# Kernel optimization log

Measured on AMD Instinct MI355X. Metric: run time of the kernel, lower is better.

Reference implementation:

```python
import jax, jax.numpy as jnp
import numpy as np

N = 262144      # active coordinates
M = 131072      # rulebook entries per kernel offset
C_IN = 64
C_OUT = 64


def setup_inputs() -> dict:
    key = jax.random.key(0)
    k1, k2, k3, k4 = jax.random.split(key, 4)
    coords = jax.random.randint(k1, (N, 3), 0, 512, dtype=jnp.int64) if jax.config.jax_enable_x64 else jax.random.randint(k1, (N, 3), 0, 512, dtype=jnp.int32)
    feats = jax.random.normal(k2, (N, C_IN), dtype=jnp.float32)
    in_rows = jax.random.randint(k3, (9, M), 0, N, dtype=jnp.int32)
    out_rows = jax.random.randint(k4, (9, M), 0, N, dtype=jnp.int32)
    # weight init matches torch: randn * (1/sqrt(in_ch))
    weight = jax.random.normal(jax.random.fold_in(key, 5), (9, C_IN, C_OUT), dtype=jnp.float32) * (1.0 / C_IN ** 0.5)
    bias = jnp.zeros((C_OUT,), dtype=jnp.float32)
    return {"coords": coords, "feats": feats, "in_rows": in_rows,
            "out_rows": out_rows, "weight": weight, "bias": bias}


def reference(coords, feats, in_rows, out_rows, weight, bias):
    # Gather input features for all 9 kernel offsets: [9, M, C_in]
    gathered = feats[in_rows]
    # Per-offset GEMM: [9, M, C_out]
    prod = jnp.einsum('kmi,kio->kmo', gathered, weight)
    # Scatter-add into output rows
    out = jnp.zeros((feats.shape[0], weight.shape[2]), dtype=feats.dtype)
    out = out.at[out_rows.reshape(-1)].add(prod.reshape(-1, weight.shape[2]))
    out = out + bias
    return (coords, out)
```

## Files before the change

kernel.cpp:

```cpp
#include <hip/hip_runtime.h>
#include <hip/hip_bf16.h>

#define NPTS 262144
#define MRB  131072
#define KOFF 9

typedef __attribute__((ext_vector_type(8))) short short8;
typedef __attribute__((ext_vector_type(4))) float f32x4;

__device__ __forceinline__ short f2bf(float f) {
    __hip_bfloat16 h = __float2bfloat16(f);
    return __builtin_bit_cast(short, h);
}

__device__ __forceinline__ void atomic_add_f32(float* p, float v) {
    __hip_atomic_fetch_add(p, v, __ATOMIC_RELAXED, __HIP_MEMORY_SCOPE_AGENT);
}

__global__ __launch_bounds__(256) void init_kernel(const int* __restrict__ coords,
                                                   const float* __restrict__ bias,
                                                   float* __restrict__ out) {
    const int tid = blockIdx.x * blockDim.x + threadIdx.x;
    const int nc4 = (NPTS * 3) / 4;
    const int nf4 = (NPTS * 64) / 4;
    for (int i = tid; i < nc4 + nf4; i += gridDim.x * blockDim.x) {
        if (i < nc4) {
            int4 c = ((const int4*)coords)[i];
            float4 f;
            f.x = (float)c.x; f.y = (float)c.y; f.z = (float)c.z; f.w = (float)c.w;
            ((float4*)out)[i] = f;
        } else {
            int j = i - nc4;
            float4 b = ((const float4*)bias)[j & 15];
            ((float4*)(out + (size_t)NPTS * 3))[j] = b;
        }
    }
}

__global__ __launch_bounds__(256) void conv_main(const float* __restrict__ feats,
                                                 const int*   __restrict__ in_rows,
                                                 const int*   __restrict__ out_rows,
                                                 const float* __restrict__ weight,
                                                 float*       __restrict__ out) {
    const int lane = threadIdx.x & 63;
    const int wv   = threadIdx.x >> 6;
    const int lrow = lane & 15;
    const int lhi  = lane >> 4;
    const int BPK  = MRB / 64;
    const int k    = blockIdx.x / BPK;
    const int mb   = (blockIdx.x % BPK) * 64 + wv * 16;

    const float* Wk = weight + k * 64 * 64;
    short8 bfrag[2][4];
#pragma unroll
    for (int kk = 0; kk < 2; ++kk)
#pragma unroll
        for (int nt = 0; nt < 4; ++nt)
#pragma unroll
            for (int j = 0; j < 8; ++j)
                bfrag[kk][nt][j] = f2bf(Wk[(kk * 32 + lhi * 8 + j) * 64 + nt * 16 + lrow]);

    const int arow = in_rows[k * MRB + mb + lrow];
    const float* ap = feats + (long)arow * 64 + lhi * 8;

    f32x4 acc[4] = {};
#pragma unroll
    for (int kk = 0; kk < 2; ++kk) {
        float4 f0 = *(const float4*)(ap + kk * 32);
        float4 f1 = *(const float4*)(ap + kk * 32 + 4);
        short8 afrag;
        afrag[0] = f2bf(f0.x); afrag[1] = f2bf(f0.y);
        afrag[2] = f2bf(f0.z); afrag[3] = f2bf(f0.w);
        afrag[4] = f2bf(f1.x); afrag[5] = f2bf(f1.y);
        afrag[6] = f2bf(f1.z); afrag[7] = f2bf(f1.w);
#pragma unroll
        for (int nt = 0; nt < 4; ++nt)
            acc[nt] = __builtin_amdgcn_mfma_f32_16x16x32_bf16(afrag, bfrag[kk][nt], acc[nt], 0, 0, 0);
    }

    const int ob = k * MRB + mb + lhi * 4;
#pragma unroll
    for (int r = 0; r < 4; ++r) {
        const int orow = out_rows[ob + r];
        float* op = out + (long)orow * 64 + lrow;
#pragma unroll
        for (int nt = 0; nt < 4; ++nt)
            atomic_add_f32(op + nt * 16, acc[nt][r]);
    }
}

extern "C" void kernel_launch(void* const* d_in, const int* in_sizes, int n_in,
                              void* d_out, int out_size, void* d_ws, size_t ws_size,
                              hipStream_t stream) {
    const int*   coords   = (const int*)  d_in[0];
    const float* feats    = (const float*)d_in[1];
    const int*   in_rows  = (const int*)  d_in[2];
    const int*   out_rows = (const int*)  d_in[3];
    const float* weight   = (const float*)d_in[4];
    const float* bias     = (const float*)d_in[5];
    float* out = (float*)d_out;

    hipLaunchKernelGGL(init_kernel, dim3(2048), dim3(256), 0, stream, coords, bias, out);
    hipLaunchKernelGGL(conv_main, dim3(KOFF * (MRB / 64)), dim3(256), 0, stream,
                       feats, in_rows, out_rows, weight, out + (size_t)NPTS * 3);
}
```

Measured before the change: 364.2 us.

## Replace float atomic scatter with counting-sort bucketing and segmented reduction

```diff
diff --git a/kernel.cpp b/kernel.cpp
--- a/kernel.cpp
+++ b/kernel.cpp
@@ -4,22 +4,182 @@
 #define NPTS 262144
 #define MRB  131072
 #define KOFF 9
+#define NENT (KOFF * MRB)
 
 typedef __attribute__((ext_vector_type(8))) short short8;
+typedef __attribute__((ext_vector_type(4))) short short4v;
 typedef __attribute__((ext_vector_type(4))) float f32x4;
 
 __device__ __forceinline__ short f2bf(float f) {
     __hip_bfloat16 h = __float2bfloat16(f);
     return __builtin_bit_cast(short, h);
 }
-
+__device__ __forceinline__ float bf2f(unsigned short u) {
+    unsigned int x = ((unsigned int)u) << 16;
+    return __builtin_bit_cast(float, x);
+}
 __device__ __forceinline__ void atomic_add_f32(float* p, float v) {
     __hip_atomic_fetch_add(p, v, __ATOMIC_RELAXED, __HIP_MEMORY_SCOPE_AGENT);
 }
 
-__global__ __launch_bounds__(256) void init_kernel(const int* __restrict__ coords,
-                                                   const float* __restrict__ bias,
-                                                   float* __restrict__ out) {
+#define PROD_OFF   0ull
+#define POS_OFF    150994944ull
+#define START_OFF  155713536ull
+#define CURSOR_OFF 156762368ull
+#define COUNTS_OFF 157810944ull
+#define BSUM_OFF   158859520ull
+#define WS_NEED    158860544ull
+
+
+__global__ __launch_bounds__(256) void init_fast(const int* __restrict__ coords,
+                                                 float* __restrict__ out,
+                                                 int* __restrict__ counts) {
+    const int i = blockIdx.x * 256 + threadIdx.x;
+    const int nc4 = (NPTS * 3) / 4;
+    if (i < nc4) {
+        int4 c = ((const int4*)coords)[i];
+        float4 f;
+        f.x = (float)c.x; f.y = (float)c.y; f.z = (float)c.z; f.w = (float)c.w;
+        ((float4*)out)[i] = f;
+    } else {
+        int j = i - nc4;
+        ((int4*)counts)[j] = make_int4(0, 0, 0, 0);
+    }
+}
+
+__global__ __launch_bounds__(256) void hist_kernel(const int* __restrict__ out_rows,
+                                                   int* __restrict__ counts) {
+    const int e = blockIdx.x * 256 + threadIdx.x;
+    atomicAdd(&counts[out_rows[e]], 1);
+}
+
+__global__ __launch_bounds__(1024) void scan_blocks(const int* __restrict__ counts,
+                                                    int* __restrict__ start,
+                                                    int* __restrict__ bsum) {
+    __shared__ int lds[1024];
+    const int tid = threadIdx.x;
+    const int gid = blockIdx.x * 1024 + tid;
+    int v = counts[gid];
+    lds[tid] = v;
+    __syncthreads();
+#pragma unroll
+    for (int off = 1; off < 1024; off <<= 1) {
+        int t = (tid >= off) ? lds[tid - off] : 0;
+        __syncthreads();
+        lds[tid] += t;
+        __syncthreads();
+    }
+    start[gid] = lds[tid] - v;
+    if (tid == 1023) bsum[blockIdx.x] = lds[tid];
+}
+
+__global__ __launch_bounds__(256) void scan_bsum(int* __restrict__ bsum) {
+    __shared__ int lds[256];
+    const int tid = threadIdx.x;
+    int v = bsum[tid];
+    lds[tid] = v;
+    __syncthreads();
+#pragma unroll
+    for (int off = 1; off < 256; off <<= 1) {
+        int t = (tid >= off) ? lds[tid - off] : 0;
+        __syncthreads();
+        lds[tid] += t;
+        __syncthreads();
+    }
+    bsum[tid] = lds[tid] - v;
+}
+
+__global__ __launch_bounds__(1024) void add_offsets(int* __restrict__ start,
+                                                    const int* __restrict__ bsum,
+                                                    int* __restrict__ cursor) {
+    const int gid = blockIdx.x * 1024 + threadIdx.x;
+    int s = start[gid] + bsum[blockIdx.x];
+    start[gid] = s;
+    cursor[gid] = s;
+    if (gid == 0) start[NPTS] = NENT;
+}
+
+__global__ __launch_bounds__(256) void fill_pos(const int* __restrict__ out_rows,
+                                                int* __restrict__ cursor,
+                                                int* __restrict__ pos) {
+    const int e = blockIdx.x * 256 + threadIdx.x;
+    pos[e] = atomicAdd(&cursor[out_rows[e]], 1);
+}
+
+__global__ __launch_bounds__(256) void conv_prod(const float* __restrict__ feats,
+                                                 const int*   __restrict__ in_rows,
+                                                 const float* __restrict__ weight,
+                                                 const int*   __restrict__ pos,
+                                                 short*       __restrict__ prod) {
+    const int lane = threadIdx.x & 63;
+    const int wv   = threadIdx.x >> 6;
+    const int lrow = lane & 15;
+    const int lhi  = lane >> 4;
+    const int BPK  = MRB / 64;
+    const int k    = blockIdx.x / BPK;
+    const int mb   = (blockIdx.x % BPK) * 64 + wv * 16;
+
+    const float* Wk = weight + k * 64 * 64;
+    short8 wfrag[2][4];
+#pragma unroll
+    for (int kk = 0; kk < 2; ++kk)
+#pragma unroll
+        for (int mt = 0; mt < 4; ++mt)
+#pragma unroll
+            for (int j = 0; j < 8; ++j)
+                wfrag[kk][mt][j] = f2bf(Wk[(kk * 32 + lhi * 8 + j) * 64 + mt * 16 + lrow]);
+
+    const int e    = k * MRB + mb + lrow;
+    const int arow = in_rows[e];
+    const float* ap = feats + (long)arow * 64 + lhi * 8;
+
+    f32x4 acc[4] = {};
+#pragma unroll
+    for (int kk = 0; kk < 2; ++kk) {
+        float4 f0 = *(const float4*)(ap + kk * 32);
+        float4 f1 = *(const float4*)(ap + kk * 32 + 4);
+        short8 ffrag;
+        ffrag[0] = f2bf(f0.x); ffrag[1] = f2bf(f0.y);
+        ffrag[2] = f2bf(f0.z); ffrag[3] = f2bf(f0.w);
+        ffrag[4] = f2bf(f1.x); ffrag[5] = f2bf(f1.y);
+        ffrag[6] = f2bf(f1.z); ffrag[7] = f2bf(f1.w);
+#pragma unroll
+        for (int mt = 0; mt < 4; ++mt)
+            acc[mt] = __builtin_amdgcn_mfma_f32_16x16x32_bf16(wfrag[kk][mt], ffrag, acc[mt], 0, 0, 0);
+    }
+
+    const int p = pos[e];
+    short* pp = prod + (size_t)p * 64 + lhi * 4;
+#pragma unroll
+    for (int mt = 0; mt < 4; ++mt) {
+        short4v s;
+        s[0] = f2bf(acc[mt][0]); s[1] = f2bf(acc[mt][1]);
+        s[2] = f2bf(acc[mt][2]); s[3] = f2bf(acc[mt][3]);
+        *(short4v*)(pp + mt * 16) = s;
+    }
+}
+
+__global__ __launch_bounds__(256) void reduce_out(const short* __restrict__ prod,
+                                                  const int*   __restrict__ start,
+                                                  const float* __restrict__ bias,
+                                                  float*       __restrict__ out) {
+    const int lane = threadIdx.x & 63;
+    const int wid  = (blockIdx.x * 256 + threadIdx.x) >> 6;
+    const int nw   = (gridDim.x * 256) >> 6;
+    const float b  = bias[lane];
+    for (int r = wid; r < NPTS; r += nw) {
+        const int s0 = start[r], s1 = start[r + 1];
+        float acc = 0.f;
+        const unsigned short* p = (const unsigned short*)prod + (size_t)s0 * 64 + lane;
+        for (int s = s0; s < s1; ++s, p += 64)
+            acc += bf2f(*p);
+        out[(size_t)r * 64 + lane] = acc + b;
+    }
+}
+
+__global__ __launch_bounds__(256) void init_full(const int* __restrict__ coords,
+                                                 const float* __restrict__ bias,
+                                                 float* __restrict__ out) {
     const int tid = blockIdx.x * blockDim.x + threadIdx.x;
     const int nc4 = (NPTS * 3) / 4;
     const int nf4 = (NPTS * 64) / 4;
@@ -37,11 +197,11 @@
     }
 }
 
-__global__ __launch_bounds__(256) void conv_main(const float* __restrict__ feats,
-                                                 const int*   __restrict__ in_rows,
-                                                 const int*   __restrict__ out_rows,
-                                                 const float* __restrict__ weight,
-                                                 float*       __restrict__ out) {
+__global__ __launch_bounds__(256) void conv_atomic(const float* __restrict__ feats,
+                                                   const int*   __restrict__ in_rows,
+                                                   const int*   __restrict__ out_rows,
+                                                   const float* __restrict__ weight,
+                                                   float*       __restrict__ out) {
     const int lane = threadIdx.x & 63;
     const int wv   = threadIdx.x >> 6;
     const int lrow = lane & 15;
@@ -98,9 +258,30 @@
     const int*   out_rows = (const int*)  d_in[3];
     const float* weight   = (const float*)d_in[4];
     const float* bias     = (const float*)d_in[5];
-    float* out = (float*)d_out;
-
-    hipLaunchKernelGGL(init_kernel, dim3(2048), dim3(256), 0, stream, coords, bias, out);
-    hipLaunchKernelGGL(conv_main, dim3(KOFF * (MRB / 64)), dim3(256), 0, stream,
-                       feats, in_rows, out_rows, weight, out + (size_t)NPTS * 3);
-}
+    float* out      = (float*)d_out;
+    float* out_feat = out + (size_t)NPTS * 3;
+
+    if (ws_size >= WS_NEED) {
+        char* ws = (char*)d_ws;
+        short* prod  = (short*)(ws + PROD_OFF);
+        int* pos     = (int*)(ws + POS_OFF);
+        int* start   = (int*)(ws + START_OFF);
+        int* cursor  = (int*)(ws + CURSOR_OFF);
+        int* counts  = (int*)(ws + COUNTS_OFF);
+        int* bsum    = (int*)(ws + BSUM_OFF);
+
+        hipLaunchKernelGGL(init_fast,   dim3(1024), dim3(256),  0, stream, coords, out, counts);
+        hipLaunchKernelGGL(hist_kernel, dim3(NENT / 256), dim3(256), 0, stream, out_rows, counts);
+        hipLaunchKernelGGL(scan_blocks, dim3(NPTS / 1024), dim3(1024), 0, stream, counts, start, bsum);
+        hipLaunchKernelGGL(scan_bsum,   dim3(1),    dim3(256),  0, stream, bsum);
+        hipLaunchKernelGGL(add_offsets, dim3(NPTS / 1024), dim3(1024), 0, stream, start, bsum, cursor);
+        hipLaunchKernelGGL(fill_pos,    dim3(NENT / 256), dim3(256), 0, stream, out_rows, cursor, pos);
+        hipLaunchKernelGGL(conv_prod,   dim3(KOFF * (MRB / 64)), dim3(256), 0, stream,
+                           feats, in_rows, weight, pos, prod);
+        hipLaunchKernelGGL(reduce_out,  dim3(2048), dim3(256),  0, stream, prod, start, bias, out_feat);
+    } else {
+        hipLaunchKernelGGL(init_full,  dim3(2048), dim3(256), 0, stream, coords, bias, out);
+        hipLaunchKernelGGL(conv_atomic, dim3(KOFF * (MRB / 64)), dim3(256), 0, stream,
+                           feats, in_rows, out_rows, weight, out_feat);
+    }
+}
```

After: 439.8 us. 20.8% more time.

## Accumulate scatter in fp16 workspace with packed atomics and pre-converted bf16 inputs

Applied to the files above, without the earlier changes.

```diff
diff --git a/kernel.cpp b/kernel.cpp
--- a/kernel.cpp
+++ b/kernel.cpp
@@ -4,22 +4,140 @@
 #define NPTS 262144
 #define MRB  131072
 #define KOFF 9
+#define NENT (KOFF * MRB)
 
 typedef __attribute__((ext_vector_type(8))) short short8;
+typedef __attribute__((ext_vector_type(4))) short short4v;
 typedef __attribute__((ext_vector_type(4))) float f32x4;
+typedef _Float16 f16;
+typedef __attribute__((ext_vector_type(2))) _Float16 half2v;
+typedef __attribute__((ext_vector_type(4))) _Float16 f16x4;
 
 __device__ __forceinline__ short f2bf(float f) {
     __hip_bfloat16 h = __float2bfloat16(f);
     return __builtin_bit_cast(short, h);
 }
-
 __device__ __forceinline__ void atomic_add_f32(float* p, float v) {
     __hip_atomic_fetch_add(p, v, __ATOMIC_RELAXED, __HIP_MEMORY_SCOPE_AGENT);
 }
 
-__global__ __launch_bounds__(256) void init_kernel(const int* __restrict__ coords,
-                                                   const float* __restrict__ bias,
-                                                   float* __restrict__ out) {
+#if __has_builtin(__builtin_amdgcn_global_atomic_fadd_v2f16)
+typedef __attribute__((address_space(1))) half2v ghalf2;
+__device__ __forceinline__ void atomic_pk_add(f16* p, float x, float y) {
+    half2v v = {(f16)x, (f16)y};
+    __builtin_amdgcn_global_atomic_fadd_v2f16((ghalf2*)p, v);
+}
+#else
+__device__ __forceinline__ void atomic_pk_add(f16* p, float x, float y) {
+    half2v v = {(f16)x, (f16)y};
+    asm volatile("global_atomic_pk_add_f16 %0, %1, off" :: "v"(p), "v"(v) : "memory");
+}
+#endif
+
+#define FB_OFF   0ull
+#define WBF_OFF  33554432ull
+#define ACC_OFF  33628160ull
+#define ACC_BYTES 33554432ull
+#define WS_NEED  67182592ull
+
+
+__global__ __launch_bounds__(256) void prep(const int*   __restrict__ coords,
+                                            const float* __restrict__ feats,
+                                            const float* __restrict__ weight,
+                                            float* __restrict__ out,
+                                            short* __restrict__ fb,
+                                            short* __restrict__ wbf) {
+    const int T0 = (NPTS * 3) / 4;
+    const int T1 = T0 + NPTS * 16;
+    const int T2 = T1 + (KOFF * 8 * 64);
+    const int stride = gridDim.x * 256;
+    for (int i = blockIdx.x * 256 + threadIdx.x; i < T2; i += stride) {
+        if (i < T0) {
+            int4 c = ((const int4*)coords)[i];
+            float4 f;
+            f.x = (float)c.x; f.y = (float)c.y; f.z = (float)c.z; f.w = (float)c.w;
+            ((float4*)out)[i] = f;
+        } else if (i < T1) {
+            int j = i - T0;
+            float4 f = ((const float4*)feats)[j];
+            short4v s;
+            s[0] = f2bf(f.x); s[1] = f2bf(f.y); s[2] = f2bf(f.z); s[3] = f2bf(f.w);
+            ((short4v*)fb)[j] = s;
+        } else {
+            int w    = i - T1;
+            int lane = w & 63;
+            int g    = w >> 6;
+            int mt   = g & 3, kk = (g >> 2) & 1, k = g >> 3;
+            int lhi  = lane >> 4, lrow = lane & 15;
+            const float* Wk = weight + k * 64 * 64;
+            short8 v;
+#pragma unroll
+            for (int j = 0; j < 8; ++j)
+                v[j] = f2bf(Wk[(kk * 32 + lhi * 8 + j) * 64 + mt * 16 + lrow]);
+            ((short8*)wbf)[g * 64 + lane] = v;
+        }
+    }
+}
+
+__global__ __launch_bounds__(256) void conv_pk(const short* __restrict__ fb,
+                                               const int*   __restrict__ in_rows,
+                                               const int*   __restrict__ out_rows,
+                                               const short* __restrict__ wbf,
+                                               f16*         __restrict__ accum) {
+    const int lane = threadIdx.x & 63;
+    const int wv   = threadIdx.x >> 6;
+    const int lrow = lane & 15;
+    const int lhi  = lane >> 4;
+    const int BPK  = MRB / 64;
+    const int k    = blockIdx.x / BPK;
+    const int mb   = (blockIdx.x % BPK) * 64 + wv * 16;
+
+    short8 wfrag[2][4];
+#pragma unroll
+    for (int kk = 0; kk < 2; ++kk)
+#pragma unroll
+        for (int mt = 0; mt < 4; ++mt)
+            wfrag[kk][mt] = ((const short8*)wbf)[(k * 8 + kk * 4 + mt) * 64 + lane];
+
+    const int e    = k * MRB + mb + lrow;
+    const int arow = in_rows[e];
+    const short* ap = fb + (size_t)arow * 64 + lhi * 8;
+
+    f32x4 acc[4] = {};
+#pragma unroll
+    for (int kk = 0; kk < 2; ++kk) {
+        short8 ffrag = *(const short8*)(ap + kk * 32);
+#pragma unroll
+        for (int mt = 0; mt < 4; ++mt)
+            acc[mt] = __builtin_amdgcn_mfma_f32_16x16x32_bf16(wfrag[kk][mt], ffrag, acc[mt], 0, 0, 0);
+    }
+
+    const int orow = out_rows[e];
+    f16* op = accum + (size_t)orow * 64 + lhi * 4;
+#pragma unroll
+    for (int mt = 0; mt < 4; ++mt) {
+        atomic_pk_add(op + mt * 16,     acc[mt][0], acc[mt][1]);
+        atomic_pk_add(op + mt * 16 + 2, acc[mt][2], acc[mt][3]);
+    }
+}
+
+__global__ __launch_bounds__(256) void finalize(const f16* __restrict__ accum,
+                                                const float* __restrict__ bias,
+                                                float* __restrict__ out) {
+    const int i = blockIdx.x * 256 + threadIdx.x;
+    f16x4 v = ((const f16x4*)accum)[i];
+    float4 b = ((const float4*)bias)[i & 15];
+    float4 o;
+    o.x = (float)v[0] + b.x;
+    o.y = (float)v[1] + b.y;
+    o.z = (float)v[2] + b.z;
+    o.w = (float)v[3] + b.w;
+    ((float4*)out)[i] = o;
+}
+
+__global__ __launch_bounds__(256) void init_full(const int* __restrict__ coords,
+                                                 const float* __restrict__ bias,
+                                                 float* __restrict__ out) {
     const int tid = blockIdx.x * blockDim.x + threadIdx.x;
     const int nc4 = (NPTS * 3) / 4;
     const int nf4 = (NPTS * 64) / 4;
@@ -37,11 +155,11 @@
     }
 }
 
-__global__ __launch_bounds__(256) void conv_main(const float* __restrict__ feats,
-                                                 const int*   __restrict__ in_rows,
-                                                 const int*   __restrict__ out_rows,
-                                                 const float* __restrict__ weight,
-                                                 float*       __restrict__ out) {
+__global__ __launch_bounds__(256) void conv_atomic(const float* __restrict__ feats,
+                                                   const int*   __restrict__ in_rows,
+                                                   const int*   __restrict__ out_rows,
+                                                   const float* __restrict__ weight,
+                                                   float*       __restrict__ out) {
     const int lane = threadIdx.x & 63;
     const int wv   = threadIdx.x >> 6;
     const int lrow = lane & 15;
@@ -98,9 +216,25 @@
     const int*   out_rows = (const int*)  d_in[3];
     const float* weight   = (const float*)d_in[4];
     const float* bias     = (const float*)d_in[5];
-    float* out = (float*)d_out;
-
-    hipLaunchKernelGGL(init_kernel, dim3(2048), dim3(256), 0, stream, coords, bias, out);
-    hipLaunchKernelGGL(conv_main, dim3(KOFF * (MRB / 64)), dim3(256), 0, stream,
-                       feats, in_rows, out_rows, weight, out + (size_t)NPTS * 3);
-}
+    float* out      = (float*)d_out;
+    float* out_feat = out + (size_t)NPTS * 3;
+
+    if (ws_size >= WS_NEED) {
+        char* ws = (char*)d_ws;
+        short* fb    = (short*)(ws + FB_OFF);
+        short* wbf   = (short*)(ws + WBF_OFF);
+        f16*   accum = (f16*)(ws + ACC_OFF);
+
+        hipMemsetAsync(accum, 0, ACC_BYTES, stream);
+        hipLaunchKernelGGL(prep,     dim3(2048), dim3(256), 0, stream,
+                           coords, feats, weight, out, fb, wbf);
+        hipLaunchKernelGGL(conv_pk,  dim3(KOFF * (MRB / 64)), dim3(256), 0, stream,
+                           fb, in_rows, out_rows, wbf, accum);
+        hipLaunchKernelGGL(finalize, dim3(NPTS / 16), dim3(256), 0, stream,
+                           accum, bias, out_feat);
+    } else {
+        hipLaunchKernelGGL(init_full,   dim3(2048), dim3(256), 0, stream, coords, bias, out);
+        hipLaunchKernelGGL(conv_atomic, dim3(KOFF * (MRB / 64)), dim3(256), 0, stream,
+                           feats, in_rows, out_rows, weight, out_feat);
+    }
+}
```

Result: slower. 635.0 us (+74.4%).
